# Kernel optimization log

Hardware: AMD Instinct MI355X
Metric: run time of the kernel (lower is better)

## Reference

```python
import jax, jax.numpy as jnp
import numpy as np

NUM_HEADS = 16
HEAD_DIM = 128
ROTARY_DIM = 32  # head_dim * rotary_pct(0.25)
ROPE_BASE = 10000.0
SCALE = HEAD_DIM ** -0.5


def _rotate_half(x):
    x1, x2 = jnp.split(x, 2, axis=-1)
    return jnp.concatenate((-x2, x1), axis=-1)


def _rope_tables(seq_len, dtype):
    inv_freq = 1.0 / (ROPE_BASE ** (jnp.arange(0, ROTARY_DIM, 2, dtype=jnp.float32) / ROTARY_DIM))
    freqs = jnp.arange(seq_len, dtype=jnp.float32)[:, None] * inv_freq[None, :]  # [S, rd/2]
    emb = jnp.concatenate((freqs, freqs), axis=-1)  # [S, rd]
    return jnp.cos(emb).astype(dtype), jnp.sin(emb).astype(dtype)


def setup_inputs() -> dict:
    key = jax.random.key(0)
    k1, k2, k3 = jax.random.split(key, 3)
    B, S, H = 2, 2048, 2048
    hidden_states = jax.random.normal(k1, (B, S, H), dtype=jnp.float32)
    attention_mask = jnp.zeros((B, 1, S, S), dtype=jnp.float32)
    Wqkv = jax.random.normal(k2, (H, 3 * H), dtype=jnp.float32) * (H ** -0.5)
    Wout = jax.random.normal(k3, (H, H), dtype=jnp.float32) * (H ** -0.5)
    return {"hidden_states": hidden_states, "attention_mask": attention_mask,
            "Wqkv": Wqkv, "Wout": Wout}


def reference(hidden_states, attention_mask, Wqkv, Wout):
    B, S, H = hidden_states.shape
    qkv = jnp.einsum('bsh,hk->bsk', hidden_states, Wqkv)  # [B,S,3H]
    q, k, v = jnp.split(qkv, 3, axis=-1)

    def to_heads(x):
        return x.reshape(B, S, NUM_HEADS, HEAD_DIM).transpose(0, 2, 1, 3)  # [B,nh,S,hd]

    q, k, v = to_heads(q), to_heads(k), to_heads(v)

    cos, sin = _rope_tables(S, hidden_states.dtype)  # [S, ROTARY_DIM]
    cos = cos[None, None, :, :]
    sin = sin[None, None, :, :]

    def rope(x):
        xr = x[..., :ROTARY_DIM]
        xr = xr * cos + _rotate_half(xr) * sin
        return jnp.concatenate((xr, x[..., ROTARY_DIM:]), axis=-1)

    q, k = rope(q), rope(k)

    scores = jnp.einsum('bhqd,bhkd->bhqk', q, k) * SCALE + attention_mask
    probs = jax.nn.softmax(scores, axis=-1)  # dropout p=0 -> identity
    ctx = jnp.einsum('bhqk,bhkd->bhqd', probs, v)
    ctx = ctx.transpose(0, 2, 1, 3).reshape(B, S, H)
    return jnp.einsum('bsh,ho->bso', ctx, Wout)
```

## Files before the change

kernel.cpp:

```cpp
#include <hip/hip_runtime.h>

typedef __attribute__((ext_vector_type(4))) float f32x4;
typedef __attribute__((ext_vector_type(8))) short s16x8;
typedef __attribute__((ext_vector_type(4))) unsigned short u16x4;
typedef __attribute__((ext_vector_type(8))) unsigned short u16x8;

#define DEVINL __device__ __forceinline__

constexpr int Bb = 2;
constexpr int Ss = 2048;
constexpr int Hh = 2048;
constexpr int NH = 16;
constexpr int HD = 128;
constexpr float ATT_SCALE = 0.08838834764831845f;
constexpr float CEXP = ATT_SCALE * 1.44269504089f;
constexpr float INV_SCALE = 11.313708498984761f;
constexpr float RAW_THR = 90.50966799f;

DEVINL unsigned short f2bf(float f) {
    unsigned u = __float_as_uint(f);
    u += 0x7FFFu + ((u >> 16) & 1u);
    return (unsigned short)(u >> 16);
}
DEVINL float bf2f(unsigned short h) { return __uint_as_float(((unsigned)h) << 16); }
DEVINL float fexp2(float x) { return __builtin_amdgcn_exp2f(x); }

DEVINL void gl16(const void* g, void* l) {
    __builtin_amdgcn_global_load_lds((const __attribute__((address_space(1))) void*)g,
                                     (__attribute__((address_space(3))) void*)l, 16, 0, 0);
}

__global__ void zero_flag_k(int* f) { if (threadIdx.x == 0) *f = 0; }

__global__ void scan_mask_k(const float* __restrict__ m, int* __restrict__ flag) {
    size_t i = ((size_t)blockIdx.x * 256 + threadIdx.x) * 4;
    f32x4 v = *(const f32x4*)(m + i);
    int any = (v[0] != 0.f) || (v[1] != 0.f) || (v[2] != 0.f) || (v[3] != 0.f);
    if (__any(any)) { if ((threadIdx.x & 63) == 0) atomicOr(flag, 1); }
}

__global__ void convH_k(const float* __restrict__ x, unsigned short* __restrict__ y) {
    size_t i = (size_t)blockIdx.x * 256 + threadIdx.x;
    f32x4 a = *(const f32x4*)(x + i * 8);
    f32x4 b = *(const f32x4*)(x + i * 8 + 4);
    u16x8 o;
    o[0] = f2bf(a[0]); o[1] = f2bf(a[1]); o[2] = f2bf(a[2]); o[3] = f2bf(a[3]);
    o[4] = f2bf(b[0]); o[5] = f2bf(b[1]); o[6] = f2bf(b[2]); o[7] = f2bf(b[3]);
    *(u16x8*)(y + i * 8) = o;
}

__global__ void convT_k(const float* __restrict__ W, unsigned short* __restrict__ Wt,
                        int R, int C) {
    __shared__ float tile[32][33];
    int c0 = blockIdx.x * 32, r0 = blockIdx.y * 32;
    int t = threadIdx.x;
    int rr = t >> 3, cc = (t & 7) * 4;
    f32x4 v = *(const f32x4*)(W + (size_t)(r0 + rr) * C + c0 + cc);
    tile[rr][cc + 0] = v[0]; tile[rr][cc + 1] = v[1];
    tile[rr][cc + 2] = v[2]; tile[rr][cc + 3] = v[3];
    __syncthreads();
    u16x4 o;
    o[0] = f2bf(tile[cc + 0][rr]); o[1] = f2bf(tile[cc + 1][rr]);
    o[2] = f2bf(tile[cc + 2][rr]); o[3] = f2bf(tile[cc + 3][rr]);
    *(u16x4*)(Wt + (size_t)(c0 + rr) * R + r0 + cc) = o;
}

template<int MODE>
__global__ __launch_bounds__(512, 2)
void gemm256_k(const unsigned short* __restrict__ A, const unsigned short* __restrict__ Bt,
               float* __restrict__ Cf, unsigned short* __restrict__ Cb,
               int M, int N, int K) {
    __shared__ char lds[131072];
    int t = threadIdx.x, w = t >> 6, ln = t & 63, lr = ln & 15, lg = ln >> 4;
    int wm = w >> 2, wn = w & 3;
    int f = blockIdx.x, cpx = gridDim.x >> 3;
    int s = (f & 7) * cpx + (f >> 3);
    int nbn = N >> 8;
    int nb = s % nbn, mb = s / nbn;
    int m0 = mb * 256, n0 = nb * 256;
    const char* Ab = (const char*)A;
    const char* Bbp = (const char*)Bt;

    f32x4 acc[8][4];
#pragma unroll
    for (int i = 0; i < 8; ++i)
#pragma unroll
        for (int j = 0; j < 4; ++j) { acc[i][j][0] = 0.f; acc[i][j][1] = 0.f; acc[i][j][2] = 0.f; acc[i][j][3] = 0.f; }

    auto STAGE = [&](int buf, int kt) {
        size_t k0 = (size_t)kt * 64;
        char* dA = lds + buf * 65536;
        char* dB = dA + 32768;
#pragma unroll
        for (int ld = 0; ld < 4; ++ld) {
            int ci = ld * 512 + t;
            int row = ci >> 3, cb = (ci & 7) << 4;
            int sc = cb ^ ((row & 7) << 4);
            gl16(Ab + ((size_t)(m0 + row) * K + k0) * 2 + sc, dA + ci * 16);
        }
#pragma unroll
        for (int ld = 0; ld < 4; ++ld) {
            int ci = ld * 512 + t;
            int row = ci >> 3, cb = (ci & 7) << 4;
            int sc = cb ^ ((row & 7) << 4);
            gl16(Bbp + ((size_t)(n0 + row) * K + k0) * 2 + sc, dB + ci * 16);
        }
    };

    const int NT = K >> 6;
    STAGE(0, 0);
    STAGE(1, 1);

    for (int it = 0; it < (NT >> 1); ++it) {
        int e = 2 * it;
#pragma unroll
        for (int half = 0; half < 2; ++half) {
            const char* Ax = lds + half * 65536;
            const char* Bx = Ax + 32768;
            asm volatile("s_waitcnt vmcnt(8)" ::: "memory");
            __builtin_amdgcn_s_barrier();
            __builtin_amdgcn_sched_barrier(0);
            s16x8 af[8], bfr[4];
#pragma unroll
            for (int i = 0; i < 8; ++i) {
                int rowa = wm * 128 + i * 16 + lr;
                af[i] = *(const s16x8*)(Ax + rowa * 128 + ((lg * 16) ^ ((rowa & 7) << 4)));
            }
#pragma unroll
            for (int j = 0; j < 4; ++j) {
                int rowb = wn * 64 + j * 16 + lr;
                bfr[j] = *(const s16x8*)(Bx + rowb * 128 + ((lg * 16) ^ ((rowb & 7) << 4)));
            }
            asm volatile("s_waitcnt lgkmcnt(0)" ::: "memory");
            __builtin_amdgcn_sched_barrier(0);
            __builtin_amdgcn_s_setprio(1);
#pragma unroll
            for (int i = 0; i < 8; ++i)
#pragma unroll
                for (int j = 0; j < 4; ++j)
                    acc[i][j] = __builtin_amdgcn_mfma_f32_16x16x32_bf16(af[i], bfr[j], acc[i][j], 0, 0, 0);
            __builtin_amdgcn_s_setprio(0);
#pragma unroll
            for (int i = 0; i < 8; ++i) {
                int rowa = wm * 128 + i * 16 + lr;
                af[i] = *(const s16x8*)(Ax + rowa * 128 + ((64 + lg * 16) ^ ((rowa & 7) << 4)));
            }
#pragma unroll
            for (int j = 0; j < 4; ++j) {
                int rowb = wn * 64 + j * 16 + lr;
                bfr[j] = *(const s16x8*)(Bx + rowb * 128 + ((64 + lg * 16) ^ ((rowb & 7) << 4)));
            }
            asm volatile("s_waitcnt lgkmcnt(0)" ::: "memory");
            __builtin_amdgcn_sched_barrier(0);
            __builtin_amdgcn_s_barrier();
            __builtin_amdgcn_sched_barrier(0);
            int stg = e + 2 + half;
            if (stg >= NT) stg -= 2;
            STAGE(half, stg);
            __builtin_amdgcn_s_setprio(1);
#pragma unroll
            for (int i = 0; i < 8; ++i)
#pragma unroll
                for (int j = 0; j < 4; ++j)
                    acc[i][j] = __builtin_amdgcn_mfma_f32_16x16x32_bf16(af[i], bfr[j], acc[i][j], 0, 0, 0);
            __builtin_amdgcn_s_setprio(0);
        }
    }

    if (MODE == 0 && n0 < 4096 && (wn & 1) == 0) {
        float invf = fexp2((float)lr * -0.83048202372f);
#pragma unroll
        for (int i = 0; i < 8; ++i)
#pragma unroll
            for (int r = 0; r < 4; ++r) {
                int srow = (m0 + wm * 128 + i * 16 + lg * 4 + r) & (Ss - 1);
                float sn, cs;
                sincosf((float)srow * invf, &sn, &cs);
                float x1 = acc[i][0][r], x2 = acc[i][1][r];
                acc[i][0][r] = x1 * cs - x2 * sn;
                acc[i][1][r] = x2 * cs + x1 * sn;
            }
    }

#pragma unroll
    for (int i = 0; i < 8; ++i)
#pragma unroll
        for (int j = 0; j < 4; ++j)
#pragma unroll
            for (int r = 0; r < 4; ++r) {
                int gr = m0 + wm * 128 + i * 16 + lg * 4 + r;
                int gc = n0 + wn * 64 + j * 16 + lr;
                float vv = acc[i][j][r];
                if (MODE == 1) Cf[(size_t)gr * N + gc] = vv;
                else           Cb[(size_t)gr * N + gc] = f2bf(vv);
            }
}

__global__ void vtrans_k(const unsigned short* __restrict__ qkv, unsigned short* __restrict__ Vt) {
    __shared__ unsigned short tile[64][40];
    int bh = blockIdx.x; int b = bh >> 4, h = bh & 15;
    int s0 = blockIdx.y * 64, d0 = blockIdx.z * 32;
    int t = threadIdx.x;
    int r = t >> 2, c8 = (t & 3) * 8;
    u16x8 v = *(const u16x8*)(qkv + ((size_t)(b * Ss + s0 + r)) * 6144 + 4096 + h * 128 + d0 + c8);
#pragma unroll
    for (int e = 0; e < 8; ++e) tile[r][c8 + e] = v[e];
    __syncthreads();
    int dr = t >> 3, sc = (t & 7) * 8;
    u16x8 o;
#pragma unroll
    for (int e = 0; e < 8; ++e) o[e] = tile[sc + e][dr];
    *(u16x8*)(Vt + ((size_t)bh * HD + d0 + dr) * Ss + s0 + sc) = o;
}

__global__ __launch_bounds__(512)
void attn_k(const unsigned short* __restrict__ qkv, const unsigned short* __restrict__ Vt,
            const float* __restrict__ mask, unsigned short* __restrict__ ctxb,
            const int* __restrict__ flag) {
    __shared__ char ldsK[64 * 256];
    __shared__ char ldsV[128 * 128];
    __shared__ unsigned short ldsP[8][1024];
    int f = blockIdx.x;
    int swzb = (f & 7) * 64 + (f >> 3);
    int bh = swzb >> 4, qt = swzb & 15;
    int b = bh >> 4, h = bh & 15;
    int t = threadIdx.x, w = t >> 6, ln = t & 63, lr = ln & 15, lg = ln >> 4;
    int useMask = *flag;
    int qw0 = qt * 128 + w * 16;
    const char* qkvB = (const char*)qkv;
    const char* VtB = (const char*)Vt;

    s16x8 qf[4];
    size_t qbase = ((size_t)(b * Ss + qw0 + lr)) * 6144 + h * 128;
#pragma unroll
    for (int kc = 0; kc < 4; ++kc) qf[kc] = *(const s16x8*)(qkv + qbase + kc * 32 + lg * 8);

    float mr = -3e38f, lsum = 0.f;
    f32x4 ctxa[8];
#pragma unroll
    for (int dn = 0; dn < 8; ++dn) { ctxa[dn][0] = 0.f; ctxa[dn][1] = 0.f; ctxa[dn][2] = 0.f; ctxa[dn][3] = 0.f; }
    const float* mrow = mask + (size_t)b * Ss * Ss;

    for (int kk0 = 0; kk0 < Ss; kk0 += 64) {
        __syncthreads();
#pragma unroll
        for (int c = 0; c < 2; ++c) {
            int ci = c * 512 + t;
            int krow = ci >> 4, kcb = (ci & 15) << 4;
            gl16(qkvB + (((size_t)(b * Ss + kk0 + krow)) * 6144 + 2048 + h * 128) * 2 + (kcb ^ ((krow & 7) << 4)),
                 ldsK + ci * 16);
            int vrow = ci >> 3, vcb = (ci & 7) << 4;
            gl16(VtB + (((size_t)(bh * 128 + vrow)) * 2048 + kk0) * 2 + (vcb ^ ((vrow & 7) << 4)),
                 ldsV + ci * 16);
        }
        __syncthreads();

        f32x4 st[4];
#pragma unroll
        for (int n = 0; n < 4; ++n) {
            f32x4 sacc = {0.f, 0.f, 0.f, 0.f};
            const char* kb = ldsK + (n * 16 + lr) * 256;
            int sw = (lr & 7) << 4;
#pragma unroll
            for (int kc = 0; kc < 4; ++kc) {
                s16x8 kf = *(const s16x8*)(kb + ((kc * 64 + lg * 16) ^ sw));
                sacc = __builtin_amdgcn_mfma_f32_16x16x32_bf16(kf, qf[kc], sacc, 0, 0, 0);
            }
            st[n] = sacc;
        }
        if (useMask) {
#pragma unroll
            for (int n = 0; n < 4; ++n)
#pragma unroll
                for (int r = 0; r < 4; ++r)
                    st[n][r] += mrow[(size_t)(qw0 + lr) * Ss + kk0 + n * 16 + lg * 4 + r] * INV_SCALE;
        }
        float pmax = st[0][0];
#pragma unroll
        for (int n = 0; n < 4; ++n)
#pragma unroll
            for (int r = 0; r < 4; ++r) pmax = fmaxf(pmax, st[n][r]);
        pmax = fmaxf(pmax, __shfl_xor(pmax, 16));
        pmax = fmaxf(pmax, __shfl_xor(pmax, 32));
        bool need = pmax > mr + RAW_THR;
        if (__any(need)) {
            float mn = fmaxf(mr, pmax);
            float al = fexp2((mr - mn) * CEXP);
            mr = mn;
            lsum *= al;
            float a0 = __shfl(al, lg * 4 + 0), a1 = __shfl(al, lg * 4 + 1);
            float a2 = __shfl(al, lg * 4 + 2), a3 = __shfl(al, lg * 4 + 3);
#pragma unroll
            for (int dn = 0; dn < 8; ++dn) {
                ctxa[dn][0] *= a0; ctxa[dn][1] *= a1; ctxa[dn][2] *= a2; ctxa[dn][3] *= a3;
            }
        }
        float mC = mr * CEXP;
        float rs = 0.f;
        u16x4 pk[4];
#pragma unroll
        for (int n = 0; n < 4; ++n)
#pragma unroll
            for (int r = 0; r < 4; ++r) {
                float p = fexp2(st[n][r] * CEXP - mC);
                rs += p;
                pk[n][r] = f2bf(p);
            }
        rs += __shfl_xor(rs, 16);
        rs += __shfl_xor(rs, 32);
        lsum += rs;
        char* pw = (char*)ldsP[w];
        int swp = (lr & 7) << 4;
#pragma unroll
        for (int n = 0; n < 4; ++n)
            *(u16x4*)(pw + lr * 128 + ((32 * n + 8 * lg) ^ swp)) = pk[n];
        asm volatile("s_waitcnt lgkmcnt(0)" ::: "memory");
        s16x8 pa[2];
#pragma unroll
        for (int c2 = 0; c2 < 2; ++c2)
            pa[c2] = *(const s16x8*)(pw + lr * 128 + ((64 * c2 + 16 * lg) ^ swp));
#pragma unroll
        for (int dn = 0; dn < 8; ++dn) {
            const char* vb = ldsV + (dn * 16 + lr) * 128;
#pragma unroll
            for (int c2 = 0; c2 < 2; ++c2) {
                s16x8 vf = *(const s16x8*)(vb + ((c2 * 64 + lg * 16) ^ swp));
                ctxa[dn] = __builtin_amdgcn_mfma_f32_16x16x32_bf16(pa[c2], vf, ctxa[dn], 0, 0, 0);
            }
        }
    }
    float l0 = 1.f / __shfl(lsum, lg * 4 + 0), l1 = 1.f / __shfl(lsum, lg * 4 + 1);
    float l2 = 1.f / __shfl(lsum, lg * 4 + 2), l3 = 1.f / __shfl(lsum, lg * 4 + 3);
#pragma unroll
    for (int dn = 0; dn < 8; ++dn) {
        size_t base = ((size_t)(b * Ss + qw0)) * Hh + h * 128 + dn * 16 + lr;
        ctxb[base + (size_t)(lg * 4 + 0) * Hh] = f2bf(ctxa[dn][0] * l0);
        ctxb[base + (size_t)(lg * 4 + 1) * Hh] = f2bf(ctxa[dn][1] * l1);
        ctxb[base + (size_t)(lg * 4 + 2) * Hh] = f2bf(ctxa[dn][2] * l2);
        ctxb[base + (size_t)(lg * 4 + 3) * Hh] = f2bf(ctxa[dn][3] * l3);
    }
}

extern "C" void kernel_launch(void* const* d_in, const int* in_sizes, int n_in,
                              void* d_out, int out_size, void* d_ws, size_t ws_size,
                              hipStream_t stream) {
    (void)in_sizes; (void)n_in; (void)out_size; (void)ws_size;
    const float* hidden = (const float*)d_in[0];
    const float* mask   = (const float*)d_in[1];
    const float* Wqkv   = (const float*)d_in[2];
    const float* Wout   = (const float*)d_in[3];
    float* out = (float*)d_out;

    char* ws = (char*)d_ws;
    size_t off = 0;
    auto alloc = [&](size_t bytes) { char* p = ws + off; off += (bytes + 255) & ~(size_t)255; return p; };
    unsigned short* hbf   = (unsigned short*)alloc((size_t)8388608 * 2);
    unsigned short* wqkvT = (unsigned short*)alloc((size_t)12582912 * 2);
    unsigned short* woutT = (unsigned short*)alloc((size_t)4194304 * 2);
    unsigned short* qkv   = (unsigned short*)alloc((size_t)25165824 * 2);
    unsigned short* Vt    = (unsigned short*)alloc((size_t)8388608 * 2);
    int* flag             = (int*)alloc(256);
    unsigned short* ctx = hbf;

    zero_flag_k<<<1, 64, 0, stream>>>(flag);
    scan_mask_k<<<2048, 256, 0, stream>>>(mask, flag);
    convH_k<<<4096, 256, 0, stream>>>(hidden, hbf);
    convT_k<<<dim3(192, 64), 256, 0, stream>>>(Wqkv, wqkvT, 2048, 6144);
    convT_k<<<dim3(64, 64), 256, 0, stream>>>(Wout, woutT, 2048, 2048);
    gemm256_k<0><<<384, 512, 0, stream>>>(hbf, wqkvT, nullptr, qkv, 4096, 6144, 2048);
    vtrans_k<<<dim3(32, 32, 4), 256, 0, stream>>>(qkv, Vt);
    attn_k<<<512, 512, 0, stream>>>(qkv, Vt, mask, ctx, flag);
    gemm256_k<1><<<128, 512, 0, stream>>>(ctx, woutT, out, nullptr, 4096, 2048, 2048);
}
```

Baseline: 315.1 us.

## Interleave GEMM global loads with MFMA phases in finer-grained pipeline

Restructures the bf16 GEMM main loop into eight phases per pair of k-tiles. Each phase loads a quarter of the A fragments plus the B fragments, issues one quarter-tile global-to-LDS load unit, and runs 16 MFMAs. The goal is to spread global loads evenly across compute and reduce stalls at barriers, compared with issuing a whole stage of loads at once. The cost is more barriers per k-tile and more delicate vmcnt bookkeeping, which risks a race if the wait counts are wrong.

```diff
diff --git a/kernel.cpp b/kernel.cpp
--- a/kernel.cpp
+++ b/kernel.cpp
@@ -64,6 +64,42 @@
     o[2] = f2bf(tile[cc + 2][rr]); o[3] = f2bf(tile[cc + 3][rr]);
     *(u16x4*)(Wt + (size_t)(c0 + rr) * R + r0 + cc) = o;
 }
+
+#define PH(buf, kh, ih, sbuf, sunit, st, vm)                                      \
+  {                                                                               \
+    const char* Ar = lds + (buf)*65536;                                           \
+    const char* Br = Ar + 32768;                                                  \
+    s16x8 af[4];                                                                  \
+    if ((ih) == 0) {                                                              \
+      _Pragma("unroll")                                                           \
+      for (int j = 0; j < 4; ++j) {                                               \
+        int row = wn*64 + j*16 + lr;                                              \
+        bfr[j] = *(const s16x8*)(Br + row*128 + (((kh)*64 + lg*16) ^ ((row&7)<<4))); \
+      }                                                                           \
+    }                                                                             \
+    _Pragma("unroll")                                                             \
+    for (int i = 0; i < 4; ++i) {                                                 \
+      int row = wm*128 + (ih)*64 + i*16 + lr;                                     \
+      af[i] = *(const s16x8*)(Ar + row*128 + (((kh)*64 + lg*16) ^ ((row&7)<<4))); \
+    }                                                                             \
+    STG(sbuf, sunit, st);                                                         \
+    __builtin_amdgcn_s_barrier();                                                 \
+    __builtin_amdgcn_sched_barrier(0);                                            \
+    asm volatile("s_waitcnt lgkmcnt(0)" ::: "memory");                            \
+    __builtin_amdgcn_sched_barrier(0);                                            \
+    __builtin_amdgcn_s_setprio(1);                                                \
+    _Pragma("unroll")                                                             \
+    for (int i = 0; i < 4; ++i)                                                   \
+      _Pragma("unroll")                                                           \
+      for (int j = 0; j < 4; ++j)                                                 \
+        acc[(ih)*4 + i][j] = __builtin_amdgcn_mfma_f32_16x16x32_bf16(             \
+            af[i], bfr[j], acc[(ih)*4 + i][j], 0, 0, 0);                          \
+    __builtin_amdgcn_s_setprio(0);                                                \
+    if ((vm) >= 0) { asm volatile("s_waitcnt vmcnt(2)" ::: "memory"); }           \
+    __builtin_amdgcn_sched_barrier(0);                                            \
+    __builtin_amdgcn_s_barrier();                                                 \
+    __builtin_amdgcn_sched_barrier(0);                                            \
+  }
 
 template<int MODE>
 __global__ __launch_bounds__(512, 2)
@@ -87,85 +123,46 @@
 #pragma unroll
         for (int j = 0; j < 4; ++j) { acc[i][j][0] = 0.f; acc[i][j][1] = 0.f; acc[i][j][2] = 0.f; acc[i][j][3] = 0.f; }
 
-    auto STAGE = [&](int buf, int kt) {
-        size_t k0 = (size_t)kt * 64;
-        char* dA = lds + buf * 65536;
-        char* dB = dA + 32768;
-#pragma unroll
-        for (int ld = 0; ld < 4; ++ld) {
-            int ci = ld * 512 + t;
-            int row = ci >> 3, cb = (ci & 7) << 4;
-            int sc = cb ^ ((row & 7) << 4);
-            gl16(Ab + ((size_t)(m0 + row) * K + k0) * 2 + sc, dA + ci * 16);
-        }
-#pragma unroll
-        for (int ld = 0; ld < 4; ++ld) {
-            int ci = ld * 512 + t;
-            int row = ci >> 3, cb = (ci & 7) << 4;
-            int sc = cb ^ ((row & 7) << 4);
-            gl16(Bbp + ((size_t)(n0 + row) * K + k0) * 2 + sc, dB + ci * 16);
+    auto STG = [&](int sbuf, int unit, int kt) {
+        int isB = unit >> 1;
+        const char* src = isB ? Bbp : Ab;
+        int rbase = isB ? n0 : m0;
+        char* reg = lds + sbuf * 65536 + isB * 32768;
+        size_t kb = ((size_t)kt * 64) * 2;
+#pragma unroll
+        for (int rr = 0; rr < 2; ++rr) {
+            int rowbase = isB ? ((unit & 1) * 128 + rr * 64)
+                              : (rr * 128 + (unit & 1) * 64);
+            int row = rowbase + (t >> 3);
+            int slot = (t & 7) ^ (row & 7);
+            gl16(src + ((size_t)(rbase + row) * K) * 2 + kb + slot * 16,
+                 reg + rowbase * 128 + t * 16);
         }
     };
 
     const int NT = K >> 6;
-    STAGE(0, 0);
-    STAGE(1, 1);
-
+    STG(0, 0, 0); STG(0, 2, 0); STG(0, 3, 0); STG(0, 1, 0);
+    STG(1, 0, 1);
+    asm volatile("s_waitcnt vmcnt(2)" ::: "memory");
+    __builtin_amdgcn_sched_barrier(0);
+    __builtin_amdgcn_s_barrier();
+    __builtin_amdgcn_sched_barrier(0);
+
+    s16x8 bfr[4];
     for (int it = 0; it < (NT >> 1); ++it) {
-        int e = 2 * it;
-#pragma unroll
-        for (int half = 0; half < 2; ++half) {
-            const char* Ax = lds + half * 65536;
-            const char* Bx = Ax + 32768;
-            asm volatile("s_waitcnt vmcnt(8)" ::: "memory");
-            __builtin_amdgcn_s_barrier();
-            __builtin_amdgcn_sched_barrier(0);
-            s16x8 af[8], bfr[4];
-#pragma unroll
-            for (int i = 0; i < 8; ++i) {
-                int rowa = wm * 128 + i * 16 + lr;
-                af[i] = *(const s16x8*)(Ax + rowa * 128 + ((lg * 16) ^ ((rowa & 7) << 4)));
-            }
-#pragma unroll
-            for (int j = 0; j < 4; ++j) {
-                int rowb = wn * 64 + j * 16 + lr;
-                bfr[j] = *(const s16x8*)(Bx + rowb * 128 + ((lg * 16) ^ ((rowb & 7) << 4)));
-            }
-            asm volatile("s_waitcnt lgkmcnt(0)" ::: "memory");
-            __builtin_amdgcn_sched_barrier(0);
-            __builtin_amdgcn_s_setprio(1);
-#pragma unroll
-            for (int i = 0; i < 8; ++i)
-#pragma unroll
-                for (int j = 0; j < 4; ++j)
-                    acc[i][j] = __builtin_amdgcn_mfma_f32_16x16x32_bf16(af[i], bfr[j], acc[i][j], 0, 0, 0);
-            __builtin_amdgcn_s_setprio(0);
-#pragma unroll
-            for (int i = 0; i < 8; ++i) {
-                int rowa = wm * 128 + i * 16 + lr;
-                af[i] = *(const s16x8*)(Ax + rowa * 128 + ((64 + lg * 16) ^ ((rowa & 7) << 4)));
-            }
-#pragma unroll
-            for (int j = 0; j < 4; ++j) {
-                int rowb = wn * 64 + j * 16 + lr;
-                bfr[j] = *(const s16x8*)(Bx + rowb * 128 + ((64 + lg * 16) ^ ((rowb & 7) << 4)));
-            }
-            asm volatile("s_waitcnt lgkmcnt(0)" ::: "memory");
-            __builtin_amdgcn_sched_barrier(0);
-            __builtin_amdgcn_s_barrier();
-            __builtin_amdgcn_sched_barrier(0);
-            int stg = e + 2 + half;
-            if (stg >= NT) stg -= 2;
-            STAGE(half, stg);
-            __builtin_amdgcn_s_setprio(1);
-#pragma unroll
-            for (int i = 0; i < 8; ++i)
-#pragma unroll
-                for (int j = 0; j < 4; ++j)
-                    acc[i][j] = __builtin_amdgcn_mfma_f32_16x16x32_bf16(af[i], bfr[j], acc[i][j], 0, 0, 0);
-            __builtin_amdgcn_s_setprio(0);
-        }
+        int e = it * 2;
+        int e2 = (e + 2 < NT) ? e + 2 : e;
+        int e3 = (e + 3 < NT) ? e + 3 : e + 1;
+        PH(0, 0, 0,  1, 2, e + 1, -1)
+        PH(0, 0, 1,  1, 3, e + 1, -1)
+        PH(0, 1, 0,  1, 1, e + 1, -1)
+        PH(0, 1, 1,  0, 0, e2,    1)
+        PH(1, 0, 0,  0, 2, e2,   -1)
+        PH(1, 0, 1,  0, 3, e2,   -1)
+        PH(1, 1, 0,  0, 1, e2,   -1)
+        PH(1, 1, 1,  1, 0, e3,    1)
     }
+    asm volatile("s_waitcnt vmcnt(0)" ::: "memory");
 
     if (MODE == 0 && n0 < 4096 && (wn & 1) == 0) {
         float invf = fexp2((float)lr * -0.83048202372f);
```

Result: no change. 317.6 us (+0.8%).
